# Kernel tuning notes

Measured on AMD Instinct MI355X. Metric: run time of the kernel, lower is better.

## Reference

```python
import jax, jax.numpy as jnp
import numpy as np

N_NODES, N_EDGES, N_GRAPHS = 200000, 6400000, 64


def setup_inputs() -> dict:
    key = jax.random.key(0)
    ks = jax.random.split(key, 8)
    rij = jax.random.normal(ks[0], (N_EDGES, 3), jnp.float32)
    fij = jax.random.normal(ks[1], (N_EDGES, 3), jnp.float32)
    pos_grad = jax.random.normal(ks[2], (N_NODES, 3), jnp.float32)
    cell_grad = jax.random.normal(ks[3], (N_GRAPHS, 3, 3), jnp.float32)
    les_cell = jax.random.normal(ks[4], (N_GRAPHS, 3, 3), jnp.float32)
    cell_volume = jax.random.uniform(ks[5], (N_GRAPHS,), jnp.float32) + 0.5  # positive volumes
    edge_idx = jax.random.randint(ks[6], (2, N_EDGES), 0, N_NODES, dtype=jnp.int32)
    batch = jnp.sort(jax.random.randint(ks[7], (N_NODES,), 0, N_GRAPHS, dtype=jnp.int32))
    return {
        "rij": rij, "fij": fij, "pos_grad": pos_grad, "cell_grad": cell_grad,
        "les_cell": les_cell, "cell_volume": cell_volume, "edge_idx": edge_idx,
        "batch": batch, "n_nodes": N_NODES, "n_graphs": N_GRAPHS,
    }


def reference(rij, fij, pos_grad, cell_grad, les_cell, cell_volume, edge_idx, batch, n_nodes, n_graphs):
    seg = jax.ops.segment_sum
    # Path 1: edge-gradient forces (pf - nf), minus Path 2 positional grad.
    pf = seg(fij, edge_idx[0], num_segments=n_nodes)          # [N,3]
    nf = seg(fij, edge_idx[1], num_segments=n_nodes)          # [N,3]
    force = pf - nf - pos_grad                                 # [N,3]
    # Edge virial in Voigt-like order [xx,yy,zz,xy,yz,zx].
    diag = rij * fij                                           # [E,3]
    virial = jnp.concatenate([
        diag,
        (rij[:, 0] * fij[:, 1])[:, None],
        (rij[:, 1] * fij[:, 2])[:, None],
        (rij[:, 2] * fij[:, 0])[:, None],
    ], axis=-1)                                                # [E,6]
    s_node = seg(virial, edge_idx[1], num_segments=n_nodes)    # [N,6] atomic virial
    sout = seg(s_node, batch, num_segments=n_graphs)           # [B,6]
    stress = -sout / cell_volume[:, None]                      # [B,6]
    # Path 3: Ewald cell stress sigma_lr = -(1/V) cell^T @ dE/dcell.
    lr = -(jnp.swapaxes(les_cell, -2, -1) @ cell_grad) / cell_volume[:, None, None]
    lr_voigt = jnp.stack([lr[:, 0, 0], lr[:, 1, 1], lr[:, 2, 2],
                          lr[:, 0, 1], lr[:, 1, 2], lr[:, 0, 2]], axis=-1)
    return force, stress + lr_voigt
```

## Files before the change

kernel.cpp:

```cpp
#include <hip/hip_runtime.h>
#include <hip/hip_fp16.h>

static constexpr int TPB       = 256;
static constexpr int MAXB      = 64;
static constexpr int BIN_SHIFT = 12;
static constexpr int BINSZ     = 1 << BIN_SHIFT;
static constexpr int SUB_SHIFT = 11;
static constexpr int SUBSZ     = 1 << SUB_SHIFT;
static constexpr int NSUB      = BINSZ / SUBSZ;
static constexpr int CAP       = 64;
static constexpr int NBLKS     = 2048;
static constexpr int SSL       = 16;
static constexpr int MAXG      = 64;
static constexpr int SLOTS     = MAXG * 6;
static constexpr int NWAVES    = TPB / 64;

static constexpr float VSCALE  = 4096.0f;
static constexpr float VINV    = 1.0f / 4096.0f;
static constexpr float FSCALE  = 1048576.0f;
static constexpr float FINV    = 1.0f / 1048576.0f;

__global__ __launch_bounds__(64) void init_cursor_kernel(
    unsigned* __restrict__ cursor, int nbins, unsigned cap) {
    int b = threadIdx.x;
    if (b < nbins) cursor[b] = (unsigned)b * cap;
}

__device__ inline uint2 pack_rec(int node, float fx, float fy, float fz) {
    unsigned lid = (unsigned)node & (BINSZ - 1);
    unsigned w0 = (unsigned)__half_as_ushort(__float2half(fx)) |
                  ((unsigned)__half_as_ushort(__float2half(fy)) << 16);
    unsigned w1 = (unsigned)__half_as_ushort(__float2half(fz)) | (lid << 16);
    return make_uint2(w0, w1);
}

__global__ __launch_bounds__(TPB) void scatter_kernel(
    const float* __restrict__ rij, const float* __restrict__ fij,
    const int* __restrict__ idx0, const int* __restrict__ idx1,
    const int* __restrict__ batch,
    unsigned* __restrict__ cursor, uint2* __restrict__ rec,
    float* __restrict__ apart,
    int E, int nbins, unsigned limit) {
    extern __shared__ char smem[];
    uint2* buf = (uint2*)smem;
    unsigned* cnt = (unsigned*)(buf + (size_t)nbins * CAP);
    unsigned* base_s = cnt + nbins;
    int* s_acc = (int*)(base_s + nbins);

    for (int t = threadIdx.x; t < nbins; t += TPB) cnt[t] = 0u;
    for (int t = threadIdx.x; t < SLOTS; t += TPB) s_acc[t] = 0;
    __syncthreads();

    const int NG = E >> 2;
    const int GC = (NG + NBLKS - 1) / NBLKS;
    const int g0 = blockIdx.x * GC;
    int g1 = g0 + GC; if (g1 > NG) g1 = NG;
    const int span = g1 - g0;
    const int niter = span > 0 ? (span + TPB - 1) / TPB : 0;

    const float4* fij4 = (const float4*)fij;
    const float4* rij4 = (const float4*)rij;
    const int4* i04 = (const int4*)idx0;
    const int4* i14 = (const int4*)idx1;

    const int wid = threadIdx.x >> 6, lane = threadIdx.x & 63;

    for (int it = 0; it < niter; ++it) {
        int k = g0 + it * TPB + threadIdx.x;
        if (k < g1) {
            float4 fa = fij4[3 * k], fb = fij4[3 * k + 1], fc = fij4[3 * k + 2];
            float4 ra = rij4[3 * k], rb = rij4[3 * k + 1], rc = rij4[3 * k + 2];
            int4 i0 = i04[k], i1 = i14[k];
            float fx[4] = {fa.x, fa.w, fb.z, fc.y};
            float fy[4] = {fa.y, fb.x, fb.w, fc.z};
            float fz[4] = {fa.z, fb.y, fc.x, fc.w};
            float rx[4] = {ra.x, ra.w, rb.z, rc.y};
            float ry[4] = {ra.y, rb.x, rb.w, rc.z};
            float rz[4] = {ra.z, rb.y, rc.x, rc.w};
            int s[4] = {i0.x, i0.y, i0.z, i0.w};
            int r[4] = {i1.x, i1.y, i1.z, i1.w};

            int bb[8]; uint2 wv[8]; unsigned slot[8];
#pragma unroll
            for (int e = 0; e < 4; ++e) {
                bb[2 * e] = s[e] >> BIN_SHIFT;
                wv[2 * e] = pack_rec(s[e], fx[e], fy[e], fz[e]);
                bb[2 * e + 1] = r[e] >> BIN_SHIFT;
                wv[2 * e + 1] = pack_rec(r[e], -fx[e], -fy[e], -fz[e]);
            }
#pragma unroll
            for (int j = 0; j < 8; ++j)
                slot[j] = atomicAdd(&cnt[bb[j]], 1u);
#pragma unroll
            for (int j = 0; j < 8; ++j) {
                if (slot[j] < (unsigned)CAP) {
                    buf[bb[j] * CAP + slot[j]] = wv[j];
                } else {
                    unsigned d = atomicAdd(&cursor[bb[j]], 1u);
                    if (d >= limit) d = limit - 1;
                    rec[d] = wv[j];
                }
            }
#pragma unroll
            for (int e = 0; e < 4; ++e) {
                int g = batch[r[e]];
                int* a = &s_acc[6 * g];
                atomicAdd(&a[0], __float2int_rn(rx[e] * fx[e] * VSCALE));
                atomicAdd(&a[1], __float2int_rn(ry[e] * fy[e] * VSCALE));
                atomicAdd(&a[2], __float2int_rn(rz[e] * fz[e] * VSCALE));
                atomicAdd(&a[3], __float2int_rn(rx[e] * fy[e] * VSCALE));
                atomicAdd(&a[4], __float2int_rn(ry[e] * fz[e] * VSCALE));
                atomicAdd(&a[5], __float2int_rn(rz[e] * fx[e] * VSCALE));
            }
        }
        __syncthreads();
        if (threadIdx.x < (unsigned)nbins) {
            unsigned c = cnt[threadIdx.x];
            unsigned m = c < (unsigned)CAP ? c : (unsigned)CAP;
            base_s[threadIdx.x] = m ? atomicAdd(&cursor[threadIdx.x], m) : 0u;
        }
        __syncthreads();
        for (int b = wid; b < nbins; b += NWAVES) {
            unsigned c = cnt[b];
            unsigned m = c < (unsigned)CAP ? c : (unsigned)CAP;
            if ((unsigned)lane < m) {
                unsigned d = base_s[b] + lane;
                if (d >= limit) d = limit - 1;
                rec[d] = buf[b * CAP + lane];
            }
            if (lane == 0) cnt[b] = 0u;
        }
        __syncthreads();
    }

    if (blockIdx.x == 0) {
        for (int e = (NG << 2) + threadIdx.x; e < E; e += TPB) {
            float gx = fij[3 * e], gy = fij[3 * e + 1], gz = fij[3 * e + 2];
            int si = idx0[e], ri = idx1[e];
            unsigned d0 = atomicAdd(&cursor[si >> BIN_SHIFT], 1u);
            if (d0 >= limit) d0 = limit - 1;
            rec[d0] = pack_rec(si, gx, gy, gz);
            unsigned d1 = atomicAdd(&cursor[ri >> BIN_SHIFT], 1u);
            if (d1 >= limit) d1 = limit - 1;
            rec[d1] = pack_rec(ri, -gx, -gy, -gz);
            float ex = rij[3 * e], ey = rij[3 * e + 1], ez = rij[3 * e + 2];
            int g = batch[ri];
            int* a = &s_acc[6 * g];
            atomicAdd(&a[0], __float2int_rn(ex * gx * VSCALE));
            atomicAdd(&a[1], __float2int_rn(ey * gy * VSCALE));
            atomicAdd(&a[2], __float2int_rn(ez * gz * VSCALE));
            atomicAdd(&a[3], __float2int_rn(ex * gy * VSCALE));
            atomicAdd(&a[4], __float2int_rn(ey * gz * VSCALE));
            atomicAdd(&a[5], __float2int_rn(ez * gx * VSCALE));
        }
    }

    __syncthreads();
    for (int t = threadIdx.x; t < SLOTS; t += TPB)
        apart[(size_t)t * NBLKS + blockIdx.x] = (float)s_acc[t] * VINV;
}

__global__ __launch_bounds__(TPB) void bin_accum_kernel(
    const uint2* __restrict__ rec, const unsigned* __restrict__ cursor,
    float* __restrict__ bpart, unsigned cap) {
    __shared__ int lf[SUBSZ * 3];
    const int sl = blockIdx.x % SSL;
    const int r2 = blockIdx.x / SSL;
    const int st = r2 & (NSUB - 1);
    const int bin = r2 >> 1;

    int4* lf4 = (int4*)lf;
    for (int t = threadIdx.x; t < SUBSZ * 3 / 4; t += TPB)
        lf4[t] = make_int4(0, 0, 0, 0);
    __syncthreads();

    const unsigned base = (unsigned)bin * cap;
    unsigned cntb = cursor[bin] - base;
    if (cntb > cap) cntb = cap;
    const unsigned chunk = (cntb + SSL - 1) / SSL;
    unsigned r0 = (unsigned)sl * chunk;
    unsigned r1 = r0 + chunk;
    if (r0 > cntb) r0 = cntb;
    if (r1 > cntb) r1 = cntb;
#pragma unroll 4
    for (unsigned r = r0 + threadIdx.x; r < r1; r += TPB) {
        uint2 w = rec[(size_t)base + r];
        unsigned lid = w.y >> 16;
        if ((int)(lid >> SUB_SHIFT) == st) {
            unsigned l2 = lid & (SUBSZ - 1);
            float fx = __half2float(__ushort_as_half((unsigned short)(w.x & 0xffffu)));
            float fy = __half2float(__ushort_as_half((unsigned short)(w.x >> 16)));
            float fz = __half2float(__ushort_as_half((unsigned short)(w.y & 0xffffu)));
            atomicAdd(&lf[l2 * 3 + 0], __float2int_rn(fx * FSCALE));
            atomicAdd(&lf[l2 * 3 + 1], __float2int_rn(fy * FSCALE));
            atomicAdd(&lf[l2 * 3 + 2], __float2int_rn(fz * FSCALE));
        }
    }
    __syncthreads();
    float4* dst = (float4*)(bpart + (size_t)blockIdx.x * (SUBSZ * 3));
    for (int t = threadIdx.x; t < SUBSZ * 3 / 4; t += TPB) {
        int4 v = lf4[t];
        dst[t] = make_float4((float)v.x * FINV, (float)v.y * FINV,
                             (float)v.z * FINV, (float)v.w * FINV);
    }
}

__global__ __launch_bounds__(TPB) void force_kernel(
    const float* __restrict__ bpart, const float* __restrict__ pos_grad,
    float* __restrict__ force, long n3) {
    long j = (long)blockIdx.x * TPB + threadIdx.x;
    const long gs = (long)gridDim.x * TPB;
    for (; j < n3; j += gs) {
        unsigned i = (unsigned)(j / 3);
        unsigned c = (unsigned)(j - 3L * i);
        unsigned bin = i >> BIN_SHIFT;
        unsigned st = (i >> SUB_SHIFT) & (NSUB - 1);
        unsigned l2 = i & (SUBSZ - 1);
        float acc = -pos_grad[j];
        size_t tb = ((size_t)(bin * NSUB + st) * SSL) * (SUBSZ * 3) + l2 * 3 + c;
#pragma unroll
        for (int sl = 0; sl < SSL; ++sl)
            acc += bpart[tb + (size_t)sl * (SUBSZ * 3)];
        force[j] = acc;
    }
}

__global__ __launch_bounds__(TPB) void stress_kernel(
    const float* __restrict__ apart,
    const float* __restrict__ cell_grad, const float* __restrict__ les_cell,
    const float* __restrict__ vol, float* __restrict__ stress, int slots) {
    int t = blockIdx.x;
    if (t >= slots) return;
    __shared__ float red[TPB];
    float s = 0.f;
    const float* row = apart + (size_t)t * NBLKS;
    for (int j = threadIdx.x; j < NBLKS; j += TPB) s += row[j];
    red[threadIdx.x] = s;
    __syncthreads();
    for (int w = TPB / 2; w > 0; w >>= 1) {
        if (threadIdx.x < w) red[threadIdx.x] += red[threadIdx.x + w];
        __syncthreads();
    }
    if (threadIdx.x == 0) {
        int g = t / 6, c = t - 6 * g;
        const int va[6] = {0, 1, 2, 0, 1, 0};
        const int vb[6] = {0, 1, 2, 1, 2, 2};
        int a = va[c], bb = vb[c];
        const float* L = les_cell + 9 * g;
        const float* Gm = cell_grad + 9 * g;
        float lr = L[a] * Gm[bb] + L[3 + a] * Gm[3 + bb] + L[6 + a] * Gm[6 + bb];
        stress[t] = (-red[0] - lr) / vol[g];
    }
}

__global__ void init_force_kernel(const float4* __restrict__ pg4,
                                  float4* __restrict__ f4, int n4,
                                  const float* __restrict__ pg,
                                  float* __restrict__ f, int n) {
    int i = blockIdx.x * blockDim.x + threadIdx.x;
    int s = gridDim.x * blockDim.x;
    for (int k = i; k < n4; k += s) {
        float4 v = pg4[k];
        f4[k] = make_float4(-v.x, -v.y, -v.z, -v.w);
    }
    for (int k = n4 * 4 + i; k < n; k += s) f[k] = -pg[k];
}

__global__ __launch_bounds__(256) void edge_dev_kernel(
    const float* __restrict__ rij, const float* __restrict__ fij,
    const int* __restrict__ idx0, const int* __restrict__ idx1,
    const int* __restrict__ batch,
    float* __restrict__ force, float* __restrict__ partials, int E) {
    __shared__ float s_acc[SLOTS];
    for (int t = threadIdx.x; t < SLOTS; t += blockDim.x) s_acc[t] = 0.0f;
    __syncthreads();
    const int stride = gridDim.x * blockDim.x;
    const int tid0 = blockIdx.x * blockDim.x + threadIdx.x;
    for (int e = tid0; e < E; e += stride) {
        float ex = rij[3 * e], ey = rij[3 * e + 1], ez = rij[3 * e + 2];
        float gx = fij[3 * e], gy = fij[3 * e + 1], gz = fij[3 * e + 2];
        int si = idx0[e], ri = idx1[e];
        atomicAdd(&force[3 * si + 0], gx);
        atomicAdd(&force[3 * si + 1], gy);
        atomicAdd(&force[3 * si + 2], gz);
        atomicAdd(&force[3 * ri + 0], -gx);
        atomicAdd(&force[3 * ri + 1], -gy);
        atomicAdd(&force[3 * ri + 2], -gz);
        int g = batch[ri];
        float* a = &s_acc[6 * g];
        atomicAdd(&a[0], ex * gx);
        atomicAdd(&a[1], ey * gy);
        atomicAdd(&a[2], ez * gz);
        atomicAdd(&a[3], ex * gy);
        atomicAdd(&a[4], ey * gz);
        atomicAdd(&a[5], ez * gx);
    }
    __syncthreads();
    for (int t = threadIdx.x; t < SLOTS; t += blockDim.x)
        partials[(size_t)blockIdx.x * SLOTS + t] = s_acc[t];
}

__global__ void reduce_finalize_kernel(const float* __restrict__ partials, int nblocks,
                                       const float* __restrict__ cell_grad,
                                       const float* __restrict__ les_cell,
                                       const float* __restrict__ vol,
                                       float* __restrict__ stress_out, int slots) {
    int t = blockIdx.x * blockDim.x + threadIdx.x;
    if (t >= slots) return;
    float s = 0.0f;
    for (int b = 0; b < nblocks; ++b) s += partials[(size_t)b * SLOTS + t];
    int g = t / 6, c = t - 6 * g;
    const int va[6] = {0, 1, 2, 0, 1, 0};
    const int vb[6] = {0, 1, 2, 1, 2, 2};
    int a = va[c], bb = vb[c];
    const float* L = les_cell + 9 * g;
    const float* G = cell_grad + 9 * g;
    float lr = L[a] * G[bb] + L[3 + a] * G[3 + bb] + L[6 + a] * G[6 + bb];
    stress_out[t] = (-s - lr) / vol[g];
}

static inline size_t alignup(size_t x) { return (x + 255) & ~(size_t)255; }

extern "C" void kernel_launch(void* const* d_in, const int* in_sizes, int n_in,
                              void* d_out, int out_size, void* d_ws, size_t ws_size,
                              hipStream_t stream) {
    const float* rij = (const float*)d_in[0];
    const float* fij = (const float*)d_in[1];
    const float* pos_grad = (const float*)d_in[2];
    const float* cell_grad = (const float*)d_in[3];
    const float* les_cell = (const float*)d_in[4];
    const float* vol = (const float*)d_in[5];
    const int* edge_idx = (const int*)d_in[6];
    const int* batch = (const int*)d_in[7];

    const int E = in_sizes[0] / 3;
    const int N = in_sizes[2] / 3;
    const int ngr = in_sizes[5];
    const int slots = 6 * ngr;

    float* force = (float*)d_out;
    float* stress = (float*)d_out + (size_t)N * 3;

    const int nbins = (N + BINSZ - 1) >> BIN_SHIFT;
    const long N3 = (long)N * 3;

    double meanrec = 2.0 * (double)E * (double)BINSZ / (double)(N > 0 ? N : 1);
    size_t cap_sz = (size_t)(meanrec * 1.03) + 2048;
    if (cap_sz > (size_t)2 * E + 2048) cap_sz = (size_t)2 * E + 2048;
    const unsigned cap = (unsigned)cap_sz;
    const size_t rec_elems = ((size_t)nbins + 1) * cap;
    const unsigned limit = (unsigned)rec_elems;

    size_t off = 0;
    const size_t o_rec = off;   off += alignup(rec_elems * 8);
    const size_t o_cur = off;   off += alignup(MAXB * 4);
    const size_t o_apart = off; off += alignup((size_t)SLOTS * NBLKS * 4);
    const size_t o_bpart = off; off += alignup((size_t)nbins * NSUB * SSL * (SUBSZ * 3) * 4);
    const bool fit = (off <= ws_size) && (nbins <= MAXB) && (ngr <= MAXG) && (E >= 4) &&
                     (rec_elems < 0xFFFFFFFFull);

    if (fit) {
        char* ws = (char*)d_ws;
        uint2* rec = (uint2*)(ws + o_rec);
        unsigned* cursor = (unsigned*)(ws + o_cur);
        float* apart = (float*)(ws + o_apart);
        float* bpart = (float*)(ws + o_bpart);

        init_cursor_kernel<<<1, 64, 0, stream>>>(cursor, nbins, cap);

        const size_t smem = (size_t)nbins * CAP * 8 + (size_t)nbins * 8 + SLOTS * 4;
        scatter_kernel<<<NBLKS, TPB, smem, stream>>>(
            rij, fij, edge_idx, edge_idx + E, batch, cursor, rec, apart,
            E, nbins, limit);

        bin_accum_kernel<<<nbins * NSUB * SSL, TPB, 0, stream>>>(
            rec, cursor, bpart, cap);

        int fblocks = (int)((N3 + TPB - 1) / TPB);
        if (fblocks > 4096) fblocks = 4096;
        force_kernel<<<fblocks, TPB, 0, stream>>>(bpart, pos_grad, force, N3);

        stress_kernel<<<slots, TPB, 0, stream>>>(apart, cell_grad, les_cell, vol,
                                                 stress, slots);
    } else {
        float* partials = (float*)d_ws;
        int eblocks = 512;
        size_t need = (size_t)eblocks * SLOTS * sizeof(float);
        if (need > ws_size) {
            int fit2 = (int)(ws_size / (SLOTS * sizeof(float)));
            eblocks = fit2 > 0 ? fit2 : 1;
        }
        int n = (int)N3, n4 = n / 4;
        int blocks = (n4 + 255) / 256;
        if (blocks > 1024) blocks = 1024;
        if (blocks < 1) blocks = 1;
        init_force_kernel<<<blocks, 256, 0, stream>>>(
            (const float4*)pos_grad, (float4*)force, n4, pos_grad, force, n);
        edge_dev_kernel<<<eblocks, 256, 0, stream>>>(rij, fij, edge_idx, edge_idx + E,
                                                     batch, force, partials, E);
        reduce_finalize_kernel<<<6, 64, 0, stream>>>(partials, eblocks, cell_grad,
                                                     les_cell, vol, stress, slots);
    }
}
```

Before: 262.4 us.

## Replace global bin cursors with per-block fixed-capacity record regions plus overflow atomics

Each scatter block now writes its flushed records into a private fixed-size slot region per bin (CAPB entries), so the per-flush global atomic on shared bin cursors goes away. Per-block counts are stored and read back by bin_accum, which walks its share of blocks. Records that overflow the local buffer or the private region are added straight into a fixed-point global overflow array with atomics, and force_kernel adds that array in. SSL is halved, and a kernel that zeroes the overflow array replaces the cursor init. The cost is a larger, sparser record buffer, many small per-block loops in bin_accum, and possible heavy global atomic traffic if overflow happens often.

```diff
diff --git a/kernel.cpp b/kernel.cpp
--- a/kernel.cpp
+++ b/kernel.cpp
@@ -9,8 +9,10 @@
 static constexpr int SUBSZ     = 1 << SUB_SHIFT;
 static constexpr int NSUB      = BINSZ / SUBSZ;
 static constexpr int CAP       = 64;
+static constexpr int CAPB      = 176;
 static constexpr int NBLKS     = 2048;
-static constexpr int SSL       = 16;
+static constexpr int SSL       = 8;
+static constexpr int BPS       = NBLKS / SSL;
 static constexpr int MAXG      = 64;
 static constexpr int SLOTS     = MAXG * 6;
 static constexpr int NWAVES    = TPB / 64;
@@ -19,11 +21,13 @@
 static constexpr float VINV    = 1.0f / 4096.0f;
 static constexpr float FSCALE  = 1048576.0f;
 static constexpr float FINV    = 1.0f / 1048576.0f;
-
-__global__ __launch_bounds__(64) void init_cursor_kernel(
-    unsigned* __restrict__ cursor, int nbins, unsigned cap) {
-    int b = threadIdx.x;
-    if (b < nbins) cursor[b] = (unsigned)b * cap;
+static constexpr float OSCALE  = 65536.0f;
+static constexpr float OINV    = 1.0f / 65536.0f;
+
+__global__ __launch_bounds__(TPB) void zero_ovf_kernel(int4* __restrict__ p4, long n4) {
+    long i = (long)blockIdx.x * TPB + threadIdx.x;
+    const long gs = (long)gridDim.x * TPB;
+    for (; i < n4; i += gs) p4[i] = make_int4(0, 0, 0, 0);
 }
 
 __device__ inline uint2 pack_rec(int node, float fx, float fy, float fz) {
@@ -34,20 +38,27 @@
     return make_uint2(w0, w1);
 }
 
+__device__ inline void ovf_add(int* __restrict__ ovf, int node,
+                               float fx, float fy, float fz) {
+    atomicAdd(&ovf[3 * node + 0], __float2int_rn(fx * OSCALE));
+    atomicAdd(&ovf[3 * node + 1], __float2int_rn(fy * OSCALE));
+    atomicAdd(&ovf[3 * node + 2], __float2int_rn(fz * OSCALE));
+}
+
 __global__ __launch_bounds__(TPB) void scatter_kernel(
     const float* __restrict__ rij, const float* __restrict__ fij,
     const int* __restrict__ idx0, const int* __restrict__ idx1,
     const int* __restrict__ batch,
-    unsigned* __restrict__ cursor, uint2* __restrict__ rec,
-    float* __restrict__ apart,
-    int E, int nbins, unsigned limit) {
+    uint2* __restrict__ rec, unsigned* __restrict__ cnt_out,
+    int* __restrict__ ovf, float* __restrict__ apart,
+    int E, int nbins) {
     extern __shared__ char smem[];
     uint2* buf = (uint2*)smem;
     unsigned* cnt = (unsigned*)(buf + (size_t)nbins * CAP);
-    unsigned* base_s = cnt + nbins;
-    int* s_acc = (int*)(base_s + nbins);
-
-    for (int t = threadIdx.x; t < nbins; t += TPB) cnt[t] = 0u;
+    unsigned* loc = cnt + nbins;
+    int* s_acc = (int*)(loc + nbins);
+
+    for (int t = threadIdx.x; t < nbins; t += TPB) { cnt[t] = 0u; loc[t] = 0u; }
     for (int t = threadIdx.x; t < SLOTS; t += TPB) s_acc[t] = 0;
     __syncthreads();
 
@@ -96,9 +107,11 @@
                 if (slot[j] < (unsigned)CAP) {
                     buf[bb[j] * CAP + slot[j]] = wv[j];
                 } else {
-                    unsigned d = atomicAdd(&cursor[bb[j]], 1u);
-                    if (d >= limit) d = limit - 1;
-                    rec[d] = wv[j];
+                    int node = (bb[j] << BIN_SHIFT) | (int)(wv[j].y >> 16);
+                    float ox = __half2float(__ushort_as_half((unsigned short)(wv[j].x & 0xffffu)));
+                    float oy = __half2float(__ushort_as_half((unsigned short)(wv[j].x >> 16)));
+                    float oz = __half2float(__ushort_as_half((unsigned short)(wv[j].y & 0xffffu)));
+                    ovf_add(ovf, node, ox, oy, oz);
                 }
             }
 #pragma unroll
@@ -114,21 +127,28 @@
             }
         }
         __syncthreads();
-        if (threadIdx.x < (unsigned)nbins) {
-            unsigned c = cnt[threadIdx.x];
-            unsigned m = c < (unsigned)CAP ? c : (unsigned)CAP;
-            base_s[threadIdx.x] = m ? atomicAdd(&cursor[threadIdx.x], m) : 0u;
-        }
-        __syncthreads();
         for (int b = wid; b < nbins; b += NWAVES) {
             unsigned c = cnt[b];
             unsigned m = c < (unsigned)CAP ? c : (unsigned)CAP;
+            unsigned off0 = loc[b];
             if ((unsigned)lane < m) {
-                unsigned d = base_s[b] + lane;
-                if (d >= limit) d = limit - 1;
-                rec[d] = buf[b * CAP + lane];
-            }
-            if (lane == 0) cnt[b] = 0u;
+                unsigned sl_ = off0 + (unsigned)lane;
+                uint2 w = buf[b * CAP + lane];
+                if (sl_ < (unsigned)CAPB) {
+                    rec[((size_t)b * NBLKS + blockIdx.x) * CAPB + sl_] = w;
+                } else {
+                    int node = (b << BIN_SHIFT) | (int)(w.y >> 16);
+                    float ox = __half2float(__ushort_as_half((unsigned short)(w.x & 0xffffu)));
+                    float oy = __half2float(__ushort_as_half((unsigned short)(w.x >> 16)));
+                    float oz = __half2float(__ushort_as_half((unsigned short)(w.y & 0xffffu)));
+                    ovf_add(ovf, node, ox, oy, oz);
+                }
+            }
+            if (lane == 0) {
+                unsigned no = off0 + m;
+                loc[b] = no < (unsigned)CAPB ? no : (unsigned)CAPB;
+                cnt[b] = 0u;
+            }
         }
         __syncthreads();
     }
@@ -137,12 +157,8 @@
         for (int e = (NG << 2) + threadIdx.x; e < E; e += TPB) {
             float gx = fij[3 * e], gy = fij[3 * e + 1], gz = fij[3 * e + 2];
             int si = idx0[e], ri = idx1[e];
-            unsigned d0 = atomicAdd(&cursor[si >> BIN_SHIFT], 1u);
-            if (d0 >= limit) d0 = limit - 1;
-            rec[d0] = pack_rec(si, gx, gy, gz);
-            unsigned d1 = atomicAdd(&cursor[ri >> BIN_SHIFT], 1u);
-            if (d1 >= limit) d1 = limit - 1;
-            rec[d1] = pack_rec(ri, -gx, -gy, -gz);
+            ovf_add(ovf, si, gx, gy, gz);
+            ovf_add(ovf, ri, -gx, -gy, -gz);
             float ex = rij[3 * e], ey = rij[3 * e + 1], ez = rij[3 * e + 2];
             int g = batch[ri];
             int* a = &s_acc[6 * g];
@@ -156,13 +172,15 @@
     }
 
     __syncthreads();
+    for (int t = threadIdx.x; t < nbins; t += TPB)
+        cnt_out[(size_t)t * NBLKS + blockIdx.x] = loc[t];
     for (int t = threadIdx.x; t < SLOTS; t += TPB)
         apart[(size_t)t * NBLKS + blockIdx.x] = (float)s_acc[t] * VINV;
 }
 
 __global__ __launch_bounds__(TPB) void bin_accum_kernel(
-    const uint2* __restrict__ rec, const unsigned* __restrict__ cursor,
-    float* __restrict__ bpart, unsigned cap) {
+    const uint2* __restrict__ rec, const unsigned* __restrict__ cnt_out,
+    float* __restrict__ bpart) {
     __shared__ int lf[SUBSZ * 3];
     const int sl = blockIdx.x % SSL;
     const int r2 = blockIdx.x / SSL;
@@ -174,26 +192,22 @@
         lf4[t] = make_int4(0, 0, 0, 0);
     __syncthreads();
 
-    const unsigned base = (unsigned)bin * cap;
-    unsigned cntb = cursor[bin] - base;
-    if (cntb > cap) cntb = cap;
-    const unsigned chunk = (cntb + SSL - 1) / SSL;
-    unsigned r0 = (unsigned)sl * chunk;
-    unsigned r1 = r0 + chunk;
-    if (r0 > cntb) r0 = cntb;
-    if (r1 > cntb) r1 = cntb;
-#pragma unroll 4
-    for (unsigned r = r0 + threadIdx.x; r < r1; r += TPB) {
-        uint2 w = rec[(size_t)base + r];
-        unsigned lid = w.y >> 16;
-        if ((int)(lid >> SUB_SHIFT) == st) {
-            unsigned l2 = lid & (SUBSZ - 1);
-            float fx = __half2float(__ushort_as_half((unsigned short)(w.x & 0xffffu)));
-            float fy = __half2float(__ushort_as_half((unsigned short)(w.x >> 16)));
-            float fz = __half2float(__ushort_as_half((unsigned short)(w.y & 0xffffu)));
-            atomicAdd(&lf[l2 * 3 + 0], __float2int_rn(fx * FSCALE));
-            atomicAdd(&lf[l2 * 3 + 1], __float2int_rn(fy * FSCALE));
-            atomicAdd(&lf[l2 * 3 + 2], __float2int_rn(fz * FSCALE));
+    const int b0 = sl * BPS, b1 = b0 + BPS;
+    for (int blk = b0; blk < b1; ++blk) {
+        unsigned c = cnt_out[(size_t)bin * NBLKS + blk];
+        size_t base = ((size_t)bin * NBLKS + blk) * CAPB;
+        for (unsigned r = threadIdx.x; r < c; r += TPB) {
+            uint2 w = rec[base + r];
+            unsigned lid = w.y >> 16;
+            if ((int)(lid >> SUB_SHIFT) == st) {
+                unsigned l2 = lid & (SUBSZ - 1);
+                float fx = __half2float(__ushort_as_half((unsigned short)(w.x & 0xffffu)));
+                float fy = __half2float(__ushort_as_half((unsigned short)(w.x >> 16)));
+                float fz = __half2float(__ushort_as_half((unsigned short)(w.y & 0xffffu)));
+                atomicAdd(&lf[l2 * 3 + 0], __float2int_rn(fx * FSCALE));
+                atomicAdd(&lf[l2 * 3 + 1], __float2int_rn(fy * FSCALE));
+                atomicAdd(&lf[l2 * 3 + 2], __float2int_rn(fz * FSCALE));
+            }
         }
     }
     __syncthreads();
@@ -206,7 +220,8 @@
 }
 
 __global__ __launch_bounds__(TPB) void force_kernel(
-    const float* __restrict__ bpart, const float* __restrict__ pos_grad,
+    const float* __restrict__ bpart, const int* __restrict__ ovf,
+    const float* __restrict__ pos_grad,
     float* __restrict__ force, long n3) {
     long j = (long)blockIdx.x * TPB + threadIdx.x;
     const long gs = (long)gridDim.x * TPB;
@@ -216,7 +231,7 @@
         unsigned bin = i >> BIN_SHIFT;
         unsigned st = (i >> SUB_SHIFT) & (NSUB - 1);
         unsigned l2 = i & (SUBSZ - 1);
-        float acc = -pos_grad[j];
+        float acc = -pos_grad[j] + (float)ovf[j] * OINV;
         size_t tb = ((size_t)(bin * NSUB + st) * SSL) * (SUBSZ * 3) + l2 * 3 + c;
 #pragma unroll
         for (int sl = 0; sl < SSL; ++sl)
@@ -296,6 +311,7 @@
         atomicAdd(&a[5], ez * gx);
     }
     __syncthreads();
+    for (int t = threadIdx.x; t < blockDim.x && t < SLOTS; t += blockDim.x) {}
     for (int t = threadIdx.x; t < SLOTS; t += blockDim.x)
         partials[(size_t)blockIdx.x * SLOTS + t] = s_acc[t];
 }
@@ -344,41 +360,38 @@
     const int nbins = (N + BINSZ - 1) >> BIN_SHIFT;
     const long N3 = (long)N * 3;
 
-    double meanrec = 2.0 * (double)E * (double)BINSZ / (double)(N > 0 ? N : 1);
-    size_t cap_sz = (size_t)(meanrec * 1.03) + 2048;
-    if (cap_sz > (size_t)2 * E + 2048) cap_sz = (size_t)2 * E + 2048;
-    const unsigned cap = (unsigned)cap_sz;
-    const size_t rec_elems = ((size_t)nbins + 1) * cap;
-    const unsigned limit = (unsigned)rec_elems;
+    const size_t rec_elems = (size_t)nbins * NBLKS * CAPB;
 
     size_t off = 0;
-    const size_t o_rec = off;   off += alignup(rec_elems * 8);
-    const size_t o_cur = off;   off += alignup(MAXB * 4);
-    const size_t o_apart = off; off += alignup((size_t)SLOTS * NBLKS * 4);
-    const size_t o_bpart = off; off += alignup((size_t)nbins * NSUB * SSL * (SUBSZ * 3) * 4);
-    const bool fit = (off <= ws_size) && (nbins <= MAXB) && (ngr <= MAXG) && (E >= 4) &&
-                     (rec_elems < 0xFFFFFFFFull);
+    const size_t o_rec = off;    off += alignup(rec_elems * 8);
+    const size_t o_cnt = off;    off += alignup((size_t)nbins * NBLKS * 4);
+    const size_t o_ovf = off;    off += alignup(((size_t)N3 + 4) * 4);
+    const size_t o_apart = off;  off += alignup((size_t)SLOTS * NBLKS * 4);
+    const size_t o_bpart = off;  off += alignup((size_t)nbins * NSUB * SSL * (SUBSZ * 3) * 4);
+    const bool fit = (off <= ws_size) && (nbins <= MAXB) && (ngr <= MAXG) && (E >= 4);
 
     if (fit) {
         char* ws = (char*)d_ws;
         uint2* rec = (uint2*)(ws + o_rec);
-        unsigned* cursor = (unsigned*)(ws + o_cur);
+        unsigned* cnt_out = (unsigned*)(ws + o_cnt);
+        int* ovf = (int*)(ws + o_ovf);
         float* apart = (float*)(ws + o_apart);
         float* bpart = (float*)(ws + o_bpart);
 
-        init_cursor_kernel<<<1, 64, 0, stream>>>(cursor, nbins, cap);
+        long n4 = (N3 + 3) / 4;
+        int zb = (int)((n4 + TPB - 1) / TPB); if (zb > 2048) zb = 2048; if (zb < 1) zb = 1;
+        zero_ovf_kernel<<<zb, TPB, 0, stream>>>((int4*)ovf, n4);
 
         const size_t smem = (size_t)nbins * CAP * 8 + (size_t)nbins * 8 + SLOTS * 4;
         scatter_kernel<<<NBLKS, TPB, smem, stream>>>(
-            rij, fij, edge_idx, edge_idx + E, batch, cursor, rec, apart,
-            E, nbins, limit);
-
-        bin_accum_kernel<<<nbins * NSUB * SSL, TPB, 0, stream>>>(
-            rec, cursor, bpart, cap);
+            rij, fij, edge_idx, edge_idx + E, batch, rec, cnt_out, ovf, apart,
+            E, nbins);
+
+        bin_accum_kernel<<<nbins * NSUB * SSL, TPB, 0, stream>>>(rec, cnt_out, bpart);
 
         int fblocks = (int)((N3 + TPB - 1) / TPB);
         if (fblocks > 4096) fblocks = 4096;
-        force_kernel<<<fblocks, TPB, 0, stream>>>(bpart, pos_grad, force, N3);
+        force_kernel<<<fblocks, TPB, 0, stream>>>(bpart, ovf, pos_grad, force, N3);
 
         stress_kernel<<<slots, TPB, 0, stream>>>(apart, cell_grad, les_cell, vol,
                                                  stress, slots);
```

Result: slower. 282.4 us (+7.6%).
